# Kernel optimization log

Hardware: AMD Instinct MI355X
Metric: run time of the kernel (lower is better)

Reference implementation:

```python
import jax, jax.numpy as jnp
import numpy as np

# TDNN with context [-2, 2], full_context=True -> kernel_width 5.
# The original per-timestep index_select + tiny conv1d loop is, for full context,
# exactly a single VALID 1D convolution over time, followed by ReLU.

B, T, D_IN, D_OUT, KW = 32, 1024, 512, 512, 5


def setup_inputs() -> dict:
    key = jax.random.key(0)
    k1, k2, k3 = jax.random.split(key, 3)
    stdv = 1.0 / np.sqrt(D_IN)
    x = jax.random.normal(k1, (B, T, D_IN), dtype=jnp.float32)
    kernel = jax.random.normal(k2, (D_OUT, D_IN, KW), dtype=jnp.float32) * stdv
    bias = jax.random.normal(k3, (D_OUT,), dtype=jnp.float32) * stdv
    return {"x": x, "kernel": kernel, "bias": bias}


def reference(x, kernel, bias):
    # x: [B, T, D_in] -> [B, D_in, T] to match torch conv1d layout
    xc = jnp.transpose(x, (0, 2, 1))
    # VALID conv over time; kernel layout OIW matches torch (out, in, width)
    out = jax.lax.conv_general_dilated(
        xc, kernel,
        window_strides=(1,),
        padding="VALID",
        dimension_numbers=("NCW", "OIW", "NCW"),
    )  # [B, D_out, T - KW + 1]
    out = out + bias[None, :, None]
    return jax.nn.relu(out)
```

## Files before the change

### kernel.cpp

```cpp
#include <hip/hip_runtime.h>
#include <stdint.h>

#define BATCH 32
#define TLEN  1024
#define DIN   512
#define DOUT  512
#define KW    5
#define TOUT  1020
#define KDIM  (DIN * KW)

#define BM 128
#define BN 128
#define BK 64

typedef __attribute__((ext_vector_type(8))) short bf16x8;
typedef __attribute__((ext_vector_type(4))) float f32x4;

__device__ __forceinline__ uint16_t f2bf(float f) {
    uint32_t u = __float_as_uint(f);
    uint32_t r = u + 0x7FFFu + ((u >> 16) & 1u);
    return (uint16_t)(r >> 16);
}

__global__ void convert_pack(const float4* __restrict__ x, uint4* __restrict__ xb,
                             const float* __restrict__ w, uint16_t* __restrict__ wb) {
    int bid = blockIdx.x;
    if (bid < 8192) {
        int idx = bid * 256 + threadIdx.x;
        float4 a = x[2 * idx];
        float4 b = x[2 * idx + 1];
        uint4 v;
        v.x = (uint32_t)f2bf(a.x) | ((uint32_t)f2bf(a.y) << 16);
        v.y = (uint32_t)f2bf(a.z) | ((uint32_t)f2bf(a.w) << 16);
        v.z = (uint32_t)f2bf(b.x) | ((uint32_t)f2bf(b.y) << 16);
        v.w = (uint32_t)f2bf(b.z) | ((uint32_t)f2bf(b.w) << 16);
        xb[idx] = v;
    } else {
        int idx = (bid - 8192) * 256 + threadIdx.x;
        int o   = idx / KDIM;
        int rem = idx - o * KDIM;
        int k   = rem >> 9;
        int i   = rem & 511;
        wb[idx] = f2bf(w[(o * DIN + i) * KW + k]);
    }
}

__global__ void __launch_bounds__(256, 4)
tdnn_gemm(const uint16_t* __restrict__ xb,
          const uint16_t* __restrict__ wb,
          const float* __restrict__ bias,
          float* __restrict__ out) {
    __shared__ uint16_t As[BM * BK];
    __shared__ uint16_t Bs[BN * BK];

    const int j    = blockIdx.x;
    const int xcd  = j & 7;
    const int nb   = (j >> 3) & 3;
    const int gi   = j >> 5;
    const int g    = gi * 8 + xcd;
    const int b    = g >> 3;
    const int tb   = g & 7;
    const int t0   = tb * BM;
    const int n0   = nb * BN;

    const int tid  = threadIdx.x;
    const int lane = tid & 63;
    const int w    = tid >> 6;
    const int m_wave = (w & 1) * 64;
    const int n_wave = (w >> 1) * 64;

    const uint16_t* xrow = xb + (size_t)b * TLEN * DIN + (size_t)t0 * DIN;
    const uint16_t* wrow = wb + (size_t)n0 * KDIM;

    f32x4 acc[4][4] = {};

    const int ml = lane & 15;
    const int kg = lane >> 4;

    for (int kb = 0; kb < KDIM; kb += BK) {
        #pragma unroll
        for (int i = 0; i < 4; ++i) {
            int c    = w * 256 + i * 64 + lane;
            int row  = c >> 3;
            int slot = c & 7;
            int ccg  = slot ^ (row & 7);
            const uint16_t* gp = xrow + row * DIN + kb + ccg * 8;
            const uint16_t* lp = &As[(w * 256 + i * 64) * 8];
            __builtin_amdgcn_global_load_lds(
                (const __attribute__((address_space(1))) void*)gp,
                (__attribute__((address_space(3))) void*)lp, 16, 0, 0);
        }
        #pragma unroll
        for (int i = 0; i < 4; ++i) {
            int c    = w * 256 + i * 64 + lane;
            int row  = c >> 3;
            int slot = c & 7;
            int ccg  = slot ^ (row & 7);
            const uint16_t* gp = wrow + (size_t)row * KDIM + kb + ccg * 8;
            const uint16_t* lp = &Bs[(w * 256 + i * 64) * 8];
            __builtin_amdgcn_global_load_lds(
                (const __attribute__((address_space(1))) void*)gp,
                (__attribute__((address_space(3))) void*)lp, 16, 0, 0);
        }
        __syncthreads();

        #pragma unroll
        for (int h = 0; h < 2; ++h) {
            const int cc = h * 4 + kg;
            bf16x8 af[4], bfr[4];
            #pragma unroll
            for (int mi = 0; mi < 4; ++mi) {
                int r = m_wave + mi * 16 + ml;
                af[mi] = *(const bf16x8*)&As[r * BK + (cc ^ (r & 7)) * 8];
            }
            #pragma unroll
            for (int ni = 0; ni < 4; ++ni) {
                int r = n_wave + ni * 16 + ml;
                bfr[ni] = *(const bf16x8*)&Bs[r * BK + (cc ^ (r & 7)) * 8];
            }
            #pragma unroll
            for (int mi = 0; mi < 4; ++mi)
                #pragma unroll
                for (int ni = 0; ni < 4; ++ni)
                    acc[mi][ni] = __builtin_amdgcn_mfma_f32_16x16x32_bf16(
                        af[mi], bfr[ni], acc[mi][ni], 0, 0, 0);
        }
        __syncthreads();
    }

    const int rq = (lane >> 4) * 4;
    #pragma unroll
    for (int ni = 0; ni < 4; ++ni) {
        int o = n0 + n_wave + ni * 16 + ml;
        float bv = bias[o];
        float* orow = out + ((size_t)b * DOUT + o) * TOUT;
        #pragma unroll
        for (int mi = 0; mi < 4; ++mi) {
            int tbase = t0 + m_wave + mi * 16 + rq;
            #pragma unroll
            for (int r = 0; r < 4; ++r) {
                int t = tbase + r;
                if (t < TOUT) {
                    float v = acc[mi][ni][r] + bv;
                    orow[t] = v > 0.0f ? v : 0.0f;
                }
            }
        }
    }
}

extern "C" void kernel_launch(void* const* d_in, const int* in_sizes, int n_in,
                              void* d_out, int out_size, void* d_ws, size_t ws_size,
                              hipStream_t stream) {
    const float* x    = (const float*)d_in[0];
    const float* wgt  = (const float*)d_in[1];
    const float* bias = (const float*)d_in[2];
    float* out = (float*)d_out;

    uint16_t* xb = (uint16_t*)d_ws;
    uint16_t* wb = (uint16_t*)((char*)d_ws + (size_t)BATCH * TLEN * DIN * 2);

    convert_pack<<<13312, 256, 0, stream>>>((const float4*)x, (uint4*)xb, wgt, wb);
    tdnn_gemm<<<1024, 256, 0, stream>>>(xb, wb, bias, out);
}
```

Baseline: 199.9 us.

## Use 256x256 tiles with 8-wave double-buffered LDS ping-pong pipeline

Enlarges the GEMM block tile to 256x256 with 512 threads and double-buffered LDS. Global-to-LDS staging for the next k-tile is interleaved with four quarter-tile MFMA phases, using explicit barriers, waitcnt and setprio. The aim is to hide load latency and raise data reuse per block. The epilogue now writes float4 vectors instead of scalars. The grid shrinks to 256 blocks, one per CU, so any imbalance or pipeline stall is no longer hidden by extra blocks.

```diff
diff --git a/kernel.cpp b/kernel.cpp
--- a/kernel.cpp
+++ b/kernel.cpp
@@ -9,9 +9,11 @@
 #define TOUT  1020
 #define KDIM  (DIN * KW)
 
-#define BM 128
-#define BN 128
+#define BM 256
+#define BN 256
 #define BK 64
+#define NT (KDIM / BK)
+#define TILE_E (BM * BK)
 
 typedef __attribute__((ext_vector_type(8))) short bf16x8;
 typedef __attribute__((ext_vector_type(4))) float f32x4;
@@ -45,105 +47,178 @@
     }
 }
 
-__global__ void __launch_bounds__(256, 4)
+
+#define STAGE_A(buf_, mh_, kt_) do {                                           \
+    const uint16_t* lb_ = As_ + (buf_) * TILE_E + (mh_) * 8192;                \
+    _Pragma("unroll")                                                          \
+    for (int ii = 0; ii < 2; ++ii) {                                          \
+        int c_  = ii * 512 + w * 64 + lane;                                   \
+        int rh_ = c_ >> 3;                                                    \
+        int g_  = (c_ & 7) ^ (rh_ & 7);                                       \
+        int gr_ = ((rh_ >> 6) << 7) + (mh_) * 64 + (rh_ & 63);                \
+        const uint16_t* gp_ = xrow + (size_t)gr_ * DIN + (kt_) * BK + g_ * 8; \
+        const uint16_t* lp_ = lb_ + (ii * 512 + w * 64) * 8;                  \
+        __builtin_amdgcn_global_load_lds(                                     \
+            (const __attribute__((address_space(1))) void*)gp_,               \
+            (__attribute__((address_space(3))) void*)lp_, 16, 0, 0);          \
+    }                                                                          \
+} while (0)
+
+#define STAGE_B(buf_, nh_, kt_) do {                                           \
+    const uint16_t* lb_ = Bs_ + (buf_) * TILE_E + (nh_) * 8192;                \
+    _Pragma("unroll")                                                          \
+    for (int ii = 0; ii < 2; ++ii) {                                          \
+        int c_  = ii * 512 + w * 64 + lane;                                   \
+        int rh_ = c_ >> 3;                                                    \
+        int g_  = (c_ & 7) ^ (rh_ & 7);                                       \
+        int gr_ = ((rh_ >> 5) << 6) + (nh_) * 32 + (rh_ & 31);                \
+        const uint16_t* gp_ = wrow + (size_t)gr_ * KDIM + (kt_) * BK + g_ * 8;\
+        const uint16_t* lp_ = lb_ + (ii * 512 + w * 64) * 8;                  \
+        __builtin_amdgcn_global_load_lds(                                     \
+            (const __attribute__((address_space(1))) void*)gp_,               \
+            (__attribute__((address_space(3))) void*)lp_, 16, 0, 0);          \
+    }                                                                          \
+} while (0)
+
+#define LDA(buf_, mh_) do {                                                    \
+    const uint16_t* Ab_ = As_ + (buf_) * TILE_E;                               \
+    _Pragma("unroll")                                                          \
+    for (int mi = 0; mi < 4; ++mi) {                                          \
+        int r_ = (mh_) * 128 + wm * 64 + mi * 16 + ml;                        \
+        _Pragma("unroll")                                                      \
+        for (int h2 = 0; h2 < 2; ++h2) {                                     \
+            int cc_ = h2 * 4 + kg;                                            \
+            af[mi][h2] = *(const bf16x8*)&Ab_[r_ * BK + ((cc_ ^ (r_ & 7)) * 8)];\
+        }                                                                      \
+    }                                                                          \
+} while (0)
+
+#define LDB(buf_, nh_) do {                                                    \
+    const uint16_t* Bb_ = Bs_ + (buf_) * TILE_E;                               \
+    _Pragma("unroll")                                                          \
+    for (int ni = 0; ni < 2; ++ni) {                                          \
+        int r_ = (nh_) * 128 + wn * 32 + ni * 16 + ml;                        \
+        _Pragma("unroll")                                                      \
+        for (int h2 = 0; h2 < 2; ++h2) {                                     \
+            int cc_ = h2 * 4 + kg;                                            \
+            bfr[ni][h2] = *(const bf16x8*)&Bb_[r_ * BK + ((cc_ ^ (r_ & 7)) * 8)];\
+        }                                                                      \
+    }                                                                          \
+} while (0)
+
+#define MMA(mh_, nh_) do {                                                     \
+    _Pragma("unroll")                                                          \
+    for (int h2 = 0; h2 < 2; ++h2)                                            \
+        _Pragma("unroll")                                                      \
+        for (int mi = 0; mi < 4; ++mi)                                        \
+            _Pragma("unroll")                                                  \
+            for (int ni = 0; ni < 2; ++ni)                                    \
+                acc[(mh_) * 4 + mi][(nh_) * 2 + ni] =                         \
+                    __builtin_amdgcn_mfma_f32_16x16x32_bf16(                  \
+                        af[mi][h2], bfr[ni][h2],                              \
+                        acc[(mh_) * 4 + mi][(nh_) * 2 + ni], 0, 0, 0);        \
+} while (0)
+
+#define BARW() do {                                                            \
+    __builtin_amdgcn_s_barrier();                                              \
+    asm volatile("s_waitcnt lgkmcnt(0)" ::: "memory");                         \
+    __builtin_amdgcn_sched_barrier(0);                                         \
+} while (0)
+
+#define DO_KTILE(BUF, KT_B, GB, KT_A, GA, VM6)                                 \
+                                                     \
+    LDA(BUF, 0); LDB(BUF, 0);                                                  \
+    if (GB) STAGE_B(1 - (BUF), 0, KT_B);                                       \
+    BARW();                                                                    \
+    __builtin_amdgcn_s_setprio(1); MMA(0, 0); __builtin_amdgcn_s_setprio(0);   \
+    __builtin_amdgcn_s_barrier();                                              \
+                                                              \
+    LDB(BUF, 1);                                                               \
+    if (GA) STAGE_A(BUF, 0, KT_A);                                             \
+    BARW();                                                                    \
+    __builtin_amdgcn_s_setprio(1); MMA(0, 1); __builtin_amdgcn_s_setprio(0);   \
+    __builtin_amdgcn_s_barrier();                                              \
+                                                              \
+    LDA(BUF, 1);                                                               \
+    if (GA) STAGE_B(BUF, 1, KT_A);                                             \
+    BARW();                                                                    \
+    __builtin_amdgcn_s_setprio(1); MMA(1, 1); __builtin_amdgcn_s_setprio(0);   \
+    __builtin_amdgcn_s_barrier();                                              \
+                                                              \
+    LDB(BUF, 0);                                                               \
+    if (GA) STAGE_A(BUF, 1, KT_A);                                             \
+    BARW();                                                                    \
+    __builtin_amdgcn_s_setprio(1); MMA(1, 0); __builtin_amdgcn_s_setprio(0);   \
+    if (VM6) { asm volatile("s_waitcnt vmcnt(6)" ::: "memory"); }              \
+    else     { asm volatile("s_waitcnt vmcnt(0)" ::: "memory"); }              \
+    __builtin_amdgcn_s_barrier();                                              \
+    __builtin_amdgcn_sched_barrier(0);
+
+__global__ void __launch_bounds__(512, 2)
 tdnn_gemm(const uint16_t* __restrict__ xb,
           const uint16_t* __restrict__ wb,
           const float* __restrict__ bias,
           float* __restrict__ out) {
-    __shared__ uint16_t As[BM * BK];
-    __shared__ uint16_t Bs[BN * BK];
-
-    const int j    = blockIdx.x;
-    const int xcd  = j & 7;
-    const int nb   = (j >> 3) & 3;
-    const int gi   = j >> 5;
-    const int g    = gi * 8 + xcd;
-    const int b    = g >> 3;
-    const int tb   = g & 7;
-    const int t0   = tb * BM;
-    const int n0   = nb * BN;
+    __shared__ uint16_t As_[2 * TILE_E];
+    __shared__ uint16_t Bs_[2 * TILE_E];
+
+    const int j  = blockIdx.x;
+    const int g  = (j & 7) * 32 + (j >> 3);
+    const int mt = g >> 1;
+    const int nt = g & 1;
+    const int b  = mt >> 2;
+    const int t0 = (mt & 3) * BM;
+    const int n0 = nt * BN;
 
     const int tid  = threadIdx.x;
     const int lane = tid & 63;
     const int w    = tid >> 6;
-    const int m_wave = (w & 1) * 64;
-    const int n_wave = (w >> 1) * 64;
+    const int wm   = w >> 2;
+    const int wn   = w & 3;
+    const int ml   = lane & 15;
+    const int kg   = lane >> 4;
 
     const uint16_t* xrow = xb + (size_t)b * TLEN * DIN + (size_t)t0 * DIN;
     const uint16_t* wrow = wb + (size_t)n0 * KDIM;
 
-    f32x4 acc[4][4] = {};
-
-    const int ml = lane & 15;
-    const int kg = lane >> 4;
-
-    for (int kb = 0; kb < KDIM; kb += BK) {
-        #pragma unroll
-        for (int i = 0; i < 4; ++i) {
-            int c    = w * 256 + i * 64 + lane;
-            int row  = c >> 3;
-            int slot = c & 7;
-            int ccg  = slot ^ (row & 7);
-            const uint16_t* gp = xrow + row * DIN + kb + ccg * 8;
-            const uint16_t* lp = &As[(w * 256 + i * 64) * 8];
-            __builtin_amdgcn_global_load_lds(
-                (const __attribute__((address_space(1))) void*)gp,
-                (__attribute__((address_space(3))) void*)lp, 16, 0, 0);
-        }
-        #pragma unroll
-        for (int i = 0; i < 4; ++i) {
-            int c    = w * 256 + i * 64 + lane;
-            int row  = c >> 3;
-            int slot = c & 7;
-            int ccg  = slot ^ (row & 7);
-            const uint16_t* gp = wrow + (size_t)row * KDIM + kb + ccg * 8;
-            const uint16_t* lp = &Bs[(w * 256 + i * 64) * 8];
-            __builtin_amdgcn_global_load_lds(
-                (const __attribute__((address_space(1))) void*)gp,
-                (__attribute__((address_space(3))) void*)lp, 16, 0, 0);
-        }
-        __syncthreads();
-
-        #pragma unroll
-        for (int h = 0; h < 2; ++h) {
-            const int cc = h * 4 + kg;
-            bf16x8 af[4], bfr[4];
-            #pragma unroll
-            for (int mi = 0; mi < 4; ++mi) {
-                int r = m_wave + mi * 16 + ml;
-                af[mi] = *(const bf16x8*)&As[r * BK + (cc ^ (r & 7)) * 8];
-            }
-            #pragma unroll
-            for (int ni = 0; ni < 4; ++ni) {
-                int r = n_wave + ni * 16 + ml;
-                bfr[ni] = *(const bf16x8*)&Bs[r * BK + (cc ^ (r & 7)) * 8];
-            }
-            #pragma unroll
-            for (int mi = 0; mi < 4; ++mi)
-                #pragma unroll
-                for (int ni = 0; ni < 4; ++ni)
-                    acc[mi][ni] = __builtin_amdgcn_mfma_f32_16x16x32_bf16(
-                        af[mi], bfr[ni], acc[mi][ni], 0, 0, 0);
-        }
-        __syncthreads();
+    f32x4 acc[8][4] = {};
+    bf16x8 af[4][2];
+    bf16x8 bfr[2][2];
+
+    STAGE_A(0, 0, 0);
+    STAGE_B(0, 0, 0);
+    STAGE_A(0, 1, 0);
+    STAGE_B(0, 1, 0);
+    STAGE_A(1, 0, 1);
+    STAGE_B(1, 1, 1);
+    STAGE_A(1, 1, 1);
+    asm volatile("s_waitcnt vmcnt(6)" ::: "memory");
+    __builtin_amdgcn_s_barrier();
+    __builtin_amdgcn_sched_barrier(0);
+
+    for (int kt = 0; kt < NT; kt += 2) {
+        const bool ga0 = (kt + 2) < NT;
+        const bool ga1 = (kt + 3) < NT;
+        DO_KTILE(0, kt + 1, true, kt + 2, ga0, ga0)
+        DO_KTILE(1, kt + 2, ga0,  kt + 3, ga1, ga1)
     }
 
     const int rq = (lane >> 4) * 4;
     #pragma unroll
-    for (int ni = 0; ni < 4; ++ni) {
-        int o = n0 + n_wave + ni * 16 + ml;
-        float bv = bias[o];
+    for (int nf = 0; nf < 4; ++nf) {
+        const int o = n0 + wn * 64 + (nf >> 1) * 32 + (nf & 1) * 16 + ml;
+        const float bv = bias[o];
         float* orow = out + ((size_t)b * DOUT + o) * TOUT;
         #pragma unroll
-        for (int mi = 0; mi < 4; ++mi) {
-            int tbase = t0 + m_wave + mi * 16 + rq;
-            #pragma unroll
-            for (int r = 0; r < 4; ++r) {
-                int t = tbase + r;
-                if (t < TOUT) {
-                    float v = acc[mi][ni][r] + bv;
-                    orow[t] = v > 0.0f ? v : 0.0f;
-                }
+        for (int mf = 0; mf < 8; ++mf) {
+            const int tb_ = t0 + wm * 128 + (mf >> 2) * 64 + (mf & 3) * 16 + rq;
+            if (tb_ + 3 < TOUT) {
+                float4 s;
+                s.x = fmaxf(acc[mf][nf][0] + bv, 0.0f);
+                s.y = fmaxf(acc[mf][nf][1] + bv, 0.0f);
+                s.z = fmaxf(acc[mf][nf][2] + bv, 0.0f);
+                s.w = fmaxf(acc[mf][nf][3] + bv, 0.0f);
+                *(float4*)(orow + tb_) = s;
             }
         }
     }
@@ -161,5 +236,5 @@
     uint16_t* wb = (uint16_t*)((char*)d_ws + (size_t)BATCH * TLEN * DIN * 2);
 
     convert_pack<<<13312, 256, 0, stream>>>((const float4*)x, (uint4*)xb, wgt, wb);
-    tdnn_gemm<<<1024, 256, 0, stream>>>(xb, wb, bias, out);
-}
+    tdnn_gemm<<<256, 512, 0, stream>>>(xb, wb, bias, out);
+}
```

After: 200.1 us. No clear change (+0.1%).
